# Performance work log

Hardware: AMD Instinct MI355X
Metric: run time of the kernel (lower is better)

The kernel has to match this reference:

```python
import jax, jax.numpy as jnp
import numpy as np

CHUNK = 32


def l2norm(x):
    return x * jax.lax.rsqrt(jnp.sum(x * x, -1, keepdims=True) + 1e-6)


def causal_dwconv(x, w):
    # x: (b, l, C), w: (C, 1, k) -- depthwise causal 1D conv (left pad k-1)
    k = w.shape[-1]
    xt = jnp.transpose(x, (0, 2, 1))
    xt = jnp.pad(xt, ((0, 0), (0, 0), (k - 1, 0)))
    y = jax.lax.conv_general_dilated(xt, w, (1,), 'VALID',
                                     dimension_numbers=('NCH', 'OIH', 'NCH'),
                                     feature_group_count=xt.shape[1])
    return jnp.transpose(y, (0, 2, 1))


def delta_rule_chunkwise(q, k, v, beta):
    # q,k: (b,h,L,dk), v: (b,h,L,dv), beta: (b,h,L). L must be divisible by CHUNK.
    b, h, L, dk = q.shape
    dv = v.shape[-1]
    n = L // CHUNK
    q = l2norm(q)
    k = l2norm(k)
    v = v * beta[..., None]
    kb = k * beta[..., None]
    resh = lambda t: t.reshape(b, h, n, CHUNK, t.shape[-1])
    q, k, v, kb = (resh(t) for t in (q, k, v, kb))
    strict = jnp.tril(jnp.ones((CHUNK, CHUNK), bool), -1)
    A = jnp.where(strict, -(kb @ jnp.swapaxes(k, -1, -2)), 0.0)
    eye = jnp.eye(CHUNK, dtype=A.dtype)
    # UT transform: the sequential forward-substitution loop computes T = (I - A)^{-1}
    T = jax.scipy.linalg.solve_triangular(eye - A, jnp.broadcast_to(eye, A.shape), lower=True)
    u = T @ v
    w = T @ kb
    incl = jnp.tril(jnp.ones((CHUNK, CHUNK), bool))  # lower incl. diag

    def step(S, xs):
        q_i, k_i, u_i, w_i = xs
        attn = jnp.where(incl, q_i @ jnp.swapaxes(k_i, -1, -2), 0.0)
        u_hat = u_i - w_i @ S
        o_i = q_i @ S + attn @ u_hat
        return S + jnp.swapaxes(k_i, -1, -2) @ u_hat, o_i

    xs = tuple(jnp.moveaxis(t, 2, 0) for t in (q, k, u, w))
    S0 = jnp.zeros((b, h, dk, dv), q.dtype)
    S, o = jax.lax.scan(step, S0, xs)
    o = jnp.moveaxis(o, 0, 2).reshape(b, h, L, dv)
    return o, S


def branch_stats(x):
    # per-head stats over the feature dim: mean, std(ddof=1), mean|x|, L2 norm
    m = jnp.mean(x, -1, keepdims=True)
    s = jnp.std(x, -1, keepdims=True, ddof=1)
    a = jnp.mean(jnp.abs(x), -1, keepdims=True)
    l = jnp.sqrt(jnp.sum(x * x, -1, keepdims=True))
    return jnp.concatenate([m, s, a, l], -1)


def reference(hidden_states, q_w, k_w, v_w, b_w, qc_w, kc_w, vc_w,
              fir_w1, fir_w3, fir_w7, fir_w31,
              mlp_w1, mlp_b1, mlp_w2, mlp_b2, gate_log_temp, onorm_w, o_w):
    B, L, D = hidden_states.shape
    H = gate_log_temp.shape[0]
    dk = q_w.shape[1] // H
    dv = v_w.shape[1] // H
    # projections + causal short conv + silu
    q = jax.nn.silu(causal_dwconv(hidden_states @ q_w, qc_w))
    k = jax.nn.silu(causal_dwconv(hidden_states @ k_w, kc_w))
    v = jax.nn.silu(causal_dwconv(hidden_states @ v_w, vc_w))
    q = q.reshape(B, L, H, dk)
    k = k.reshape(B, L, H, dk)
    v_direct = v.reshape(B, L, H, dv)
    beta = jax.nn.sigmoid(hidden_states @ b_w)  # (B,L,H)
    delta_out, _ = delta_rule_chunkwise(
        jnp.transpose(q, (0, 2, 1, 3)), jnp.transpose(k, (0, 2, 1, 3)),
        jnp.transpose(v_direct, (0, 2, 1, 3)), jnp.transpose(beta, (0, 2, 1)))
    delta_out = jnp.transpose(delta_out, (0, 2, 1, 3))  # (B,L,H,dv)
    # multi-scale depthwise FIR branches on v
    v_flat = v_direct.reshape(B, L, H * dv)
    firs = [causal_dwconv(v_flat, w).reshape(B, L, H, dv)
            for w in (fir_w1, fir_w3, fir_w7, fir_w31)]
    branches = firs + [delta_out, v_direct]  # num_streams = 6
    S = len(branches)
    stats = jnp.concatenate([branch_stats(x) for x in branches], -1)  # (B,L,H,S*4)
    gate_in = jnp.concatenate([hidden_states, stats.reshape(B, L, H * S * 4)], -1)
    hgate = jax.nn.gelu(gate_in @ mlp_w1 + mlp_b1, approximate=False)
    logits = (hgate @ mlp_w2 + mlp_b2).reshape(B, L, H, S)
    temp = jax.nn.softplus(gate_log_temp) + 0.5  # min_gate_temp = 0.5
    weights = jax.nn.softmax(logits / temp[None, None, :, None], axis=-1)
    fused = sum(weights[..., i, None] * br for i, br in enumerate(branches))
    # RMSNorm over head_v_dim (eps=1e-5)
    fused = fused * jax.lax.rsqrt(jnp.mean(fused * fused, -1, keepdims=True) + 1e-5) * onorm_w
    return fused.reshape(B, L, H * dv) @ o_w


def setup_inputs() -> dict:
    key = jax.random.key(0)
    B, L, D, H = 2, 2048, 1024, 4
    dk = dv = D // H
    S = 6
    ks = iter(jax.random.split(key, 32))
    nrm = lambda shape, s=0.02: jax.random.normal(next(ks), shape, jnp.float32) * s

    def fir(kw):
        # delta init (last tap = 1) plus small noise
        base = jnp.zeros((H * dv, 1, kw), jnp.float32).at[:, 0, -1].set(1.0)
        return base + nrm((H * dv, 1, kw))

    gate_in_dim = D + S * 4 * H  # 1120
    hgd = D * 2 // 2             # 1024
    b2 = np.zeros(H * S, np.float32)
    for h in range(H):
        b2[h * S + S - 1] = 2.0  # value_bias_init on direct-value stream
    return {
        'hidden_states': jax.random.normal(next(ks), (B, L, D), jnp.float32),
        'q_w': nrm((D, D)), 'k_w': nrm((D, D)), 'v_w': nrm((D, D)),
        'b_w': nrm((D, H)),
        'qc_w': nrm((D, 1, 4), 0.3), 'kc_w': nrm((D, 1, 4), 0.3), 'vc_w': nrm((D, 1, 4), 0.3),
        'fir_w1': fir(1), 'fir_w3': fir(3), 'fir_w7': fir(7), 'fir_w31': fir(31),
        'mlp_w1': nrm((gate_in_dim, hgd)), 'mlp_b1': jnp.zeros((hgd,), jnp.float32),
        'mlp_w2': nrm((hgd, H * S)), 'mlp_b2': jnp.asarray(b2),
        'gate_log_temp': jnp.zeros((H,), jnp.float32),
        'onorm_w': jnp.ones((dv,), jnp.float32),
        'o_w': nrm((D, D)),
    }
```

## Files before the change

### kernel.cpp

```cpp
#include <hip/hip_runtime.h>
#include <hip/hip_bf16.h>
#include <math.h>

#define B_ 2
#define L_ 2048
#define D_ 1024
#define H_ 4
#define NC 64

typedef unsigned short ushort_t;
typedef __bf16 bf16x8 __attribute__((ext_vector_type(8)));
typedef float f32x4 __attribute__((ext_vector_type(4)));
typedef ushort_t u16x8 __attribute__((ext_vector_type(8)));

__device__ __forceinline__ ushort_t f2bs(float f) {
    __hip_bfloat16 h = __float2bfloat16(f);
    ushort_t u;
    __builtin_memcpy(&u, &h, 2);
    return u;
}

__device__ __forceinline__ float wred(float v) {
    v += __shfl_down(v, 32);
    v += __shfl_down(v, 16);
    v += __shfl_down(v, 8);
    v += __shfl_down(v, 4);
    v += __shfl_down(v, 2);
    v += __shfl_down(v, 1);
    return v;
}

__device__ __forceinline__ void gload16(const void* g, void* l) {
    __builtin_amdgcn_global_load_lds((const __attribute__((address_space(1))) void*)g,
                                     (__attribute__((address_space(3))) void*)l, 16, 0, 0);
}

#define LGKM0_BAR()                                          \
    do {                                                     \
        asm volatile("s_waitcnt lgkmcnt(0)" ::: "memory");   \
        __builtin_amdgcn_s_barrier();                        \
    } while (0)

__global__ __launch_bounds__(256) void tcast_k(const float* __restrict__ W,
                                               ushort_t* __restrict__ WT, int K, int N) {
    __shared__ float tile[32 * 33];
    const int k0 = blockIdx.y << 5, n0 = blockIdx.x << 5;
    for (int e = threadIdx.x; e < 1024; e += 256)
        tile[(e >> 5) * 33 + (e & 31)] = W[(size_t)(k0 + (e >> 5)) * N + n0 + (e & 31)];
    __syncthreads();
    for (int e = threadIdx.x; e < 1024; e += 256)
        WT[(size_t)(n0 + (e >> 5)) * K + k0 + (e & 31)] = f2bs(tile[(e & 31) * 33 + (e >> 5)]);
}

__global__ __launch_bounds__(256) void cast_k(const float* __restrict__ x,
                                              ushort_t* __restrict__ y) {
    const int i = blockIdx.x * 256 + threadIdx.x;
    const float4 v = *(const float4*)&x[(size_t)i * 4];
    ushort4 p;
    p.x = f2bs(v.x); p.y = f2bs(v.y); p.z = f2bs(v.z); p.w = f2bs(v.w);
    *(ushort4*)&y[(size_t)i * 4] = p;
}

template <int ACT>
__global__ __launch_bounds__(256) void gemm_bf(const ushort_t* __restrict__ A,
                                               const ushort_t* __restrict__ Bt,
                                               const float* __restrict__ bias,
                                               float* __restrict__ C,
                                               int M, int N, int K) {
    __shared__ ushort_t As[128 * 32];
    __shared__ ushort_t Bs[128 * 32];
    const int t = threadIdx.x;
    const int wv = t >> 6, l = t & 63;
    const int m0 = blockIdx.y << 7, n0 = blockIdx.x << 7;
    const int wm = wv & 1, wn = wv >> 1;
    const int q4 = l >> 4, c16 = l & 15;
    f32x4 acc[4][4];
#pragma unroll
    for (int i = 0; i < 4; ++i)
#pragma unroll
        for (int j = 0; j < 4; ++j) {
            f32x4 z = {0.f, 0.f, 0.f, 0.f};
            acc[i][j] = z;
        }
    const int srow = (l >> 2);
    const int scol = (l & 3) << 3;
    for (int k0 = 0; k0 < K; k0 += 32) {
        __syncthreads();
#pragma unroll
        for (int si = 0; si < 2; ++si) {
            const int s = wv * 2 + si;
            gload16(&A[(size_t)(m0 + s * 16 + srow) * K + k0 + scol], &As[s * 512]);
            gload16(&Bt[(size_t)(n0 + s * 16 + srow) * K + k0 + scol], &Bs[s * 512]);
        }
        __syncthreads();
        bf16x8 af[4], bff[4];
#pragma unroll
        for (int mi = 0; mi < 4; ++mi)
            af[mi] = *(const bf16x8*)&As[(wm * 64 + mi * 16 + c16) * 32 + q4 * 8];
#pragma unroll
        for (int ni = 0; ni < 4; ++ni)
            bff[ni] = *(const bf16x8*)&Bs[(wn * 64 + ni * 16 + c16) * 32 + q4 * 8];
#pragma unroll
        for (int mi = 0; mi < 4; ++mi)
#pragma unroll
            for (int ni = 0; ni < 4; ++ni)
                acc[mi][ni] = __builtin_amdgcn_mfma_f32_16x16x32_bf16(af[mi], bff[ni],
                                                                     acc[mi][ni], 0, 0, 0);
    }
#pragma unroll
    for (int mi = 0; mi < 4; ++mi)
#pragma unroll
        for (int ni = 0; ni < 4; ++ni)
#pragma unroll
            for (int r = 0; r < 4; ++r) {
                const int row = m0 + wm * 64 + mi * 16 + q4 * 4 + r;
                const int col = n0 + wn * 64 + ni * 16 + c16;
                float v = acc[mi][ni][r];
                if (ACT == 1) {
                    v += bias[col];
                    v = 0.5f * v * (1.0f + erff(v * 0.70710678118654752f));
                }
                C[(size_t)row * N + col] = v;
            }
}

template <int DO_NORM, int EMIT_F32, int EMIT_BF>
__global__ __launch_bounds__(256) void convql_k(const float* __restrict__ X,
                                                const float* __restrict__ cw,
                                                float* __restrict__ Y,
                                                ushort_t* __restrict__ Ybf) {
    __shared__ float xs[35 * 256];
    const int bid = blockIdx.x;
    const int h = bid & 3, lt = (bid >> 2) & 63, b = bid >> 8;
    const int t = threadIdx.x;
    const int l0 = lt << 5;
    const int cg = (h << 8) | t;
    for (int e = t; e < 35 * 256; e += 256) {
        const int r = e >> 8, c = e & 255;
        const int gl = l0 + r - 3;
        xs[e] = (gl >= 0) ? X[((size_t)(b * L_) + gl) * 3072 + (h << 8) + c] : 0.f;
    }
    const float w0 = cw[cg * 4 + 0], w1 = cw[cg * 4 + 1];
    const float w2 = cw[cg * 4 + 2], w3 = cw[cg * 4 + 3];
    __syncthreads();
    float yr[32];
#pragma unroll
    for (int l = 0; l < 32; ++l) {
        const float a = xs[(l + 0) * 256 + t] * w0 + xs[(l + 1) * 256 + t] * w1 +
                        xs[(l + 2) * 256 + t] * w2 + xs[(l + 3) * 256 + t] * w3;
        yr[l] = a / (1.f + expf(-a));
    }
    if (DO_NORM) {
        __syncthreads();
#pragma unroll
        for (int l = 0; l < 32; ++l) xs[l * 256 + t] = yr[l];
        __syncthreads();
        const int wv = t >> 6, lane = t & 63;
#pragma unroll
        for (int ri = 0; ri < 8; ++ri) {
            const int r = wv * 8 + ri;
            float4 v = *(float4*)&xs[r * 256 + lane * 4];
            float ss = v.x * v.x + v.y * v.y + v.z * v.z + v.w * v.w;
            ss = wred(ss);
            ss = __shfl(ss, 0);
            const float s = rsqrtf(ss + 1e-6f);
            v.x *= s; v.y *= s; v.z *= s; v.w *= s;
            const size_t go = ((size_t)(b * L_) + l0 + r) * 1024 + (h << 8) + lane * 4;
            if (EMIT_F32) *(float4*)&Y[go] = v;
            if (EMIT_BF) {
                ushort4 p;
                p.x = f2bs(v.x); p.y = f2bs(v.y); p.z = f2bs(v.z); p.w = f2bs(v.w);
                *(ushort4*)&Ybf[go] = p;
            }
        }
    } else {
#pragma unroll
        for (int l = 0; l < 32; ++l)
            if (EMIT_F32) Y[((size_t)(b * L_) + l0 + l) * 1024 + cg] = yr[l];
    }
}

__global__ __launch_bounds__(256) void fir_k(const float* __restrict__ V,
                                             const float* __restrict__ w1w,
                                             const float* __restrict__ w3w,
                                             const float* __restrict__ w7w,
                                             const float* __restrict__ w31w,
                                             float* __restrict__ o1,
                                             float* __restrict__ o3,
                                             float* __restrict__ o7,
                                             float* __restrict__ o31) {
    __shared__ float xs[62 * 256];
    const int bid = blockIdx.x;
    const int h = bid & 3, lt = (bid >> 2) & 63, b = bid >> 8;
    const int t = threadIdx.x;
    const int l0 = lt << 5;
    const int cg = (h << 8) | t;
    for (int e = t; e < 62 * 256; e += 256) {
        const int r = e >> 8, c = e & 255;
        const int gl = l0 + r - 30;
        xs[e] = (gl >= 0) ? V[((size_t)(b * L_) + gl) * 1024 + (h << 8) + c] : 0.f;
    }
    float lw31[31], lw7[7], lw3[3];
#pragma unroll
    for (int j = 0; j < 31; ++j) lw31[j] = w31w[cg * 31 + j];
#pragma unroll
    for (int j = 0; j < 7; ++j) lw7[j] = w7w[cg * 7 + j];
#pragma unroll
    for (int j = 0; j < 3; ++j) lw3[j] = w3w[cg * 3 + j];
    const float lw1 = w1w[cg];
    __syncthreads();
    for (int l = 0; l < 32; ++l) {
        float a31 = 0.f, a7 = 0.f, a3 = 0.f, v = 0.f;
#pragma unroll
        for (int j = 0; j < 31; ++j) {
            v = xs[(l + j) * 256 + t];
            a31 += v * lw31[j];
            if (j >= 24) a7 += v * lw7[j - 24];
            if (j >= 28) a3 += v * lw3[j - 28];
        }
        const size_t go = ((size_t)(b * L_) + l0 + l) * 1024 + cg;
        o31[go] = a31;
        o7[go] = a7;
        o3[go] = a3;
        o1[go] = v * lw1;
    }
}

__global__ __launch_bounds__(64) void beta_k(const float* __restrict__ hs,
                                             const float* __restrict__ bw,
                                             float* __restrict__ beta,
                                             ushort_t* __restrict__ gin) {
    const int row = blockIdx.x;
    const int lane = threadIdx.x;
    float a0 = 0, a1 = 0, a2 = 0, a3 = 0;
    const float* hp = hs + (size_t)row * D_;
    ushort_t* gp = gin + (size_t)row * 1120;
    for (int c = lane; c < D_; c += 64) {
        const float x = hp[c];
        gp[c] = f2bs(x);
        a0 += x * bw[c * 4 + 0];
        a1 += x * bw[c * 4 + 1];
        a2 += x * bw[c * 4 + 2];
        a3 += x * bw[c * 4 + 3];
    }
    a0 = wred(a0); a1 = wred(a1); a2 = wred(a2); a3 = wred(a3);
    if (lane == 0) {
        float* o = beta + (size_t)row * 4;
        o[0] = 1.f / (1.f + expf(-a0));
        o[1] = 1.f / (1.f + expf(-a1));
        o[2] = 1.f / (1.f + expf(-a2));
        o[3] = 1.f / (1.f + expf(-a3));
    }
}

__global__ __launch_bounds__(256) void prep2_k(const ushort_t* __restrict__ qbf,
                                               const ushort_t* __restrict__ kbf,
                                               const float* __restrict__ vg,
                                               const float* __restrict__ beta,
                                               ushort_t* __restrict__ qfr,
                                               ushort_t* __restrict__ wfr,
                                               float* __restrict__ ufr,
                                               ushort_t* __restrict__ atfr,
                                               ushort_t* __restrict__ ktfr) {
    __shared__ ushort_t k_lds[32 * 264];
    __shared__ ushort_t kT_lds[256 * 32];
    __shared__ ushort_t vT_lds[256 * 32];
    __shared__ float Am[32 * 33];
    __shared__ float Tm[32 * 33];
    __shared__ ushort_t Tb[32 * 40];
    __shared__ ushort_t at_s[32 * 40];
    __shared__ float beta_s[32];
    const int bid = blockIdx.x;
    const int bh = bid >> 6, ci = bid & 63;
    const int b = bh >> 2, h = bh & 3;
    const int t = threadIdx.x;
    const int wv = t >> 6, lane = t & 63;
    const int mi = wv & 1, ni = wv >> 1;
    const int l16 = lane & 15, quad = lane >> 4;
    const size_t cb = (size_t)bid;
    const size_t grow = ((size_t)(b * L_ + ci * 32)) * 1024 + (h << 8);
    const f32x4 z4 = {0.f, 0.f, 0.f, 0.f};

    if (t < 32) beta_s[t] = beta[(size_t)(b * L_ + ci * 32 + t) * 4 + h];
#pragma unroll
    for (int j = 0; j < 4; ++j) {
        const int idx = j * 2048 + t * 8, r = idx >> 8, c = idx & 255;
        *(u16x8*)&k_lds[r * 264 + c] = *(const u16x8*)&kbf[grow + (size_t)r * 1024 + c];
    }
#pragma unroll
    for (int j = 0; j < 8; ++j) {
        const int e = j * 1024 + t * 4, r = e >> 8, c = e & 255;
        const float4 v4 = *(const float4*)&vg[grow + (size_t)r * 1024 + c];
        const float vv[4] = {v4.x, v4.y, v4.z, v4.w};
#pragma unroll
        for (int x = 0; x < 4; ++x) {
            const int cc = c + x;
            const int sp = (r >> 3) ^ ((cc >> 1) & 3);
            vT_lds[cc * 32 + sp * 8 + (r & 7)] = f2bs(vv[x]);
        }
    }
    f32x4 g = z4, atv = z4;
#pragma unroll
    for (int s = 0; s < 8; ++s) {
        const bf16x8 a =
            *(const bf16x8*)&kbf[grow + (size_t)(mi * 16 + l16) * 1024 + s * 32 + (quad << 3)];
        const bf16x8 bb =
            *(const bf16x8*)&kbf[grow + (size_t)(ni * 16 + l16) * 1024 + s * 32 + (quad << 3)];
        const bf16x8 qa =
            *(const bf16x8*)&qbf[grow + (size_t)(mi * 16 + l16) * 1024 + s * 32 + (quad << 3)];
        g = __builtin_amdgcn_mfma_f32_16x16x32_bf16(a, bb, g, 0, 0, 0);
        atv = __builtin_amdgcn_mfma_f32_16x16x32_bf16(qa, bb, atv, 0, 0, 0);
        if (ni == 0) *(bf16x8*)&qfr[((cb * 2 + mi) * 8 + s) * 512 + lane * 8] = qa;
    }
    __syncthreads();
#pragma unroll
    for (int r = 0; r < 4; ++r) {
        const int row = mi * 16 + (quad << 2) + r;
        const int col = ni * 16 + l16;
        Am[row * 33 + col] = (col < row) ? -beta_s[row] * g[r] : 0.f;
        Tm[row * 33 + col] = (row == col) ? 1.f : 0.f;
        at_s[row * 40 + col] = (col <= row) ? f2bs(atv[r]) : (ushort_t)0;
    }
#pragma unroll
    for (int j = 0; j < 8; ++j) {
        const int e = j * 1024 + t * 4, r = e >> 8, c = e & 255;
#pragma unroll
        for (int x = 0; x < 4; ++x) {
            const int cc = c + x;
            const int sp = (r >> 3) ^ ((cc >> 1) & 3);
            kT_lds[cc * 32 + sp * 8 + (r & 7)] = k_lds[r * 264 + cc];
        }
    }
    __syncthreads();
    if (wv < 2) {
        const u16x8 av = *(const u16x8*)&at_s[(wv * 16 + l16) * 40 + (quad << 3)];
        *(u16x8*)&atfr[(cb * 2 + wv) * 512 + lane * 8] = av;
    }
#pragma unroll
    for (int j2 = 0; j2 < 4; ++j2) {
        const int tc = wv * 4 + j2;
        const int c = tc * 16 + l16;
        const int sp = quad ^ ((c >> 1) & 3);
        *(u16x8*)&ktfr[(cb * 16 + tc) * 512 + lane * 8] = *(const u16x8*)&kT_lds[c * 32 + sp * 8];
    }
    for (int i = 1; i < 32; ++i) {
        if (t < 32) {
            float s = 0.f;
            for (int j = 0; j < i; ++j) s += Am[i * 33 + j] * Tm[j * 33 + t];
            Tm[i * 33 + t] += s;
        }
        __syncthreads();
    }
#pragma unroll
    for (int j = 0; j < 4; ++j) {
        const int e = j * 256 + t, i = e >> 5, jj = e & 31;
        Tb[i * 40 + jj] = f2bs(Tm[i * 33 + jj] * beta_s[jj]);
    }
    __syncthreads();
    const bf16x8 tf = *(const bf16x8*)&Tb[(mi * 16 + l16) * 40 + (quad << 3)];
#pragma unroll
    for (int j = 0; j < 8; ++j) {
        const int nt = ni * 8 + j;
        const int d = (nt << 4) + l16;
        const int sp = quad ^ ((d >> 1) & 3);
        const bf16x8 kb = *(const bf16x8*)&kT_lds[d * 32 + (sp << 3)];
        const bf16x8 vb = *(const bf16x8*)&vT_lds[d * 32 + (sp << 3)];
        const f32x4 wacc = __builtin_amdgcn_mfma_f32_16x16x32_bf16(tf, kb, z4, 0, 0, 0);
        const f32x4 uacc = __builtin_amdgcn_mfma_f32_16x16x32_bf16(tf, vb, z4, 0, 0, 0);
        *(float4*)&ufr[((cb * 16 + nt) * 2 + mi) * 256 + lane * 4] =
            make_float4(uacc[0], uacc[1], uacc[2], uacc[3]);
#pragma unroll
        for (int r = 0; r < 4; ++r) {
            const int row = mi * 16 + (quad << 2) + r;
            k_lds[row * 264 + d] = f2bs(wacc[r]);
        }
    }
    __syncthreads();
    if (wv < 2) {
#pragma unroll
        for (int s = 0; s < 8; ++s) {
            const u16x8 wv8 = *(const u16x8*)&k_lds[(wv * 16 + l16) * 264 + s * 32 + (quad << 3)];
            *(u16x8*)&wfr[((cb * 2 + wv) * 8 + s) * 512 + lane * 8] = wv8;
        }
    }
}

__global__ __launch_bounds__(256, 1) void scan5_k(const ushort_t* __restrict__ qfr,
                                                  const ushort_t* __restrict__ wfr,
                                                  const float* __restrict__ ufr,
                                                  const ushort_t* __restrict__ atfr,
                                                  const ushort_t* __restrict__ ktfr,
                                                  float* __restrict__ dlt) {
    __shared__ ushort_t uh_lds[16 * 40];
    __shared__ ushort_t S_lds[2][16 * 264];
    const int t = threadIdx.x;
    const int wv = t >> 6, lane = t & 63;
    const int bh = blockIdx.x & 7, tile = blockIdx.x >> 3;
    const int b = bh >> 2, h = bh & 3;
    const int l16 = lane & 15, quad = lane >> 4;
    for (int e = t; e < 16 * 264; e += 256) S_lds[0][e] = 0;

    f32x4 Sacc[8];
#pragma unroll
    for (int j = 0; j < 8; ++j) {
        f32x4 z = {0.f, 0.f, 0.f, 0.f};
        Sacc[j] = z;
    }

    bf16x8 wfA[8], qfA[8], atfA, ktA[8];
    bf16x8 wfB[8], qfB[8], atfB, ktB[8];
    float uvA[4], uvB[4];

    auto loadf = [&](int ci, bf16x8* wf, bf16x8* qf, bf16x8& atf, float* uv, bf16x8* ktf) {
        const size_t cb = (size_t)(bh * NC + ci);
        if (wv < 2) {
            const ushort_t* wsrc = wfr + (cb * 2 + wv) * 8 * 512;
            const ushort_t* qsrc = qfr + (cb * 2 + wv) * 8 * 512;
#pragma unroll
            for (int s = 0; s < 8; ++s) {
                wf[s] = *(const bf16x8*)&wsrc[s * 512 + lane * 8];
                qf[s] = *(const bf16x8*)&qsrc[s * 512 + lane * 8];
            }
            atf = *(const bf16x8*)&atfr[(cb * 2 + wv) * 512 + lane * 8];
            const float4 u4 = *(const float4*)&ufr[((cb * 16 + tile) * 2 + wv) * 256 + lane * 4];
            uv[0] = u4.x; uv[1] = u4.y; uv[2] = u4.z; uv[3] = u4.w;
        } else {
            const ushort_t* ksrc = ktfr + cb * 16 * 512;
#pragma unroll
            for (int j = 0; j < 8; ++j) {
                const int tc = ((wv - 2) << 3) + j;
                ktf[j] = *(const bf16x8*)&ksrc[tc * 512 + lane * 8];
            }
        }
    };
    auto sfrag = [&](int p, int k0) -> bf16x8 {
        return *(const bf16x8*)&S_lds[p][l16 * 264 + k0 + (quad << 3)];
    };
    auto uhfrag = [&]() -> bf16x8 {
        return *(const bf16x8*)&uh_lds[l16 * 40 + (quad << 3)];
    };
    auto compute = [&](int ci, bf16x8* wf, bf16x8* qf, bf16x8& atf, float* uv, bf16x8* ktf) {
        const int p = ci & 1;
        const size_t gbase = ((size_t)(b * L_ + ci * 32)) * D_ + (h << 8);
        if (wv < 2) {
            f32x4 a0 = {0.f, 0.f, 0.f, 0.f}, a1 = {0.f, 0.f, 0.f, 0.f};
#pragma unroll
            for (int s = 0; s < 8; s += 2) {
                a0 = __builtin_amdgcn_mfma_f32_16x16x32_bf16(wf[s], sfrag(p, s * 32), a0, 0, 0, 0);
                a1 = __builtin_amdgcn_mfma_f32_16x16x32_bf16(wf[s + 1], sfrag(p, s * 32 + 32), a1,
                                                             0, 0, 0);
            }
            ushort4 up;
            up.x = f2bs(uv[0] - a0[0] - a1[0]);
            up.y = f2bs(uv[1] - a0[1] - a1[1]);
            up.z = f2bs(uv[2] - a0[2] - a1[2]);
            up.w = f2bs(uv[3] - a0[3] - a1[3]);
            *(ushort4*)&uh_lds[l16 * 40 + (wv << 4) + (quad << 2)] = up;
        }
        LGKM0_BAR();
        if (wv < 2) {
            f32x4 o0 = {0.f, 0.f, 0.f, 0.f}, o1 = {0.f, 0.f, 0.f, 0.f};
#pragma unroll
            for (int s = 0; s < 8; s += 2) {
                o0 = __builtin_amdgcn_mfma_f32_16x16x32_bf16(qf[s], sfrag(p, s * 32), o0, 0, 0, 0);
                o1 = __builtin_amdgcn_mfma_f32_16x16x32_bf16(qf[s + 1], sfrag(p, s * 32 + 32), o1,
                                                             0, 0, 0);
            }
            o0 = __builtin_amdgcn_mfma_f32_16x16x32_bf16(atf, uhfrag(), o0, 0, 0, 0);
#pragma unroll
            for (int r = 0; r < 4; ++r)
                dlt[gbase + (size_t)((wv << 4) + (quad << 2) + r) * D_ + (tile << 4) + l16] =
                    o0[r] + o1[r];
        } else {
            const bf16x8 uf = uhfrag();
#pragma unroll
            for (int j = 0; j < 8; ++j)
                Sacc[j] = __builtin_amdgcn_mfma_f32_16x16x32_bf16(ktf[j], uf, Sacc[j], 0, 0, 0);
#pragma unroll
            for (int j = 0; j < 8; ++j) {
                const int c0 = ((((wv - 2) << 3) + j) << 4) + (quad << 2);
                ushort4 pk;
                pk.x = f2bs(Sacc[j][0]);
                pk.y = f2bs(Sacc[j][1]);
                pk.z = f2bs(Sacc[j][2]);
                pk.w = f2bs(Sacc[j][3]);
                *(ushort4*)&S_lds[p ^ 1][l16 * 264 + c0] = pk;
            }
        }
        LGKM0_BAR();
    };

    loadf(0, wfA, qfA, atfA, uvA, ktA);
    LGKM0_BAR();
    for (int ci = 0; ci < NC; ci += 2) {
        loadf(ci + 1, wfB, qfB, atfB, uvB, ktB);
        compute(ci, wfA, qfA, atfA, uvA, ktA);
        if (ci + 2 < NC) loadf(ci + 2, wfA, qfA, atfA, uvA, ktA);
        compute(ci + 1, wfB, qfB, atfB, uvB, ktB);
    }
}

__global__ __launch_bounds__(64) void stats_k(const float* __restrict__ f1,
                                              const float* __restrict__ f3,
                                              const float* __restrict__ f7,
                                              const float* __restrict__ f31,
                                              const float* __restrict__ dl,
                                              const float* __restrict__ vv,
                                              ushort_t* __restrict__ gin) {
    const int row = blockIdx.x;
    const int lane = threadIdx.x;
    const float* ptrs[6] = {f1, f3, f7, f31, dl, vv};
    const size_t base = (size_t)row * 256;
    ushort_t* gp = gin + (size_t)(row >> 2) * 1120 + 1024 + (row & 3) * 24;
    for (int br = 0; br < 6; ++br) {
        const float4 x = *(const float4*)&ptrs[br][base + lane * 4];
        float s1 = x.x + x.y + x.z + x.w;
        float s2 = x.x * x.x + x.y * x.y + x.z * x.z + x.w * x.w;
        float sa = fabsf(x.x) + fabsf(x.y) + fabsf(x.z) + fabsf(x.w);
        s1 = wred(s1); s2 = wred(s2); sa = wred(sa);
        if (lane == 0) {
            const float m = s1 / 256.f;
            float var = (s2 - 256.f * m * m) / 255.f;
            if (var < 0.f) var = 0.f;
            gp[br * 4 + 0] = f2bs(m);
            gp[br * 4 + 1] = f2bs(sqrtf(var));
            gp[br * 4 + 2] = f2bs(sa / 256.f);
            gp[br * 4 + 3] = f2bs(sqrtf(s2));
        }
    }
}

__global__ __launch_bounds__(256) void wts_k(const float* __restrict__ hg,
                                             const float* __restrict__ w2,
                                             const float* __restrict__ b2,
                                             const float* __restrict__ glt,
                                             float* __restrict__ wts) {
    const int row = blockIdx.x;
    const int h = threadIdx.x >> 6, lane = threadIdx.x & 63;
    float hv[16];
    const float* hp = hg + (size_t)row * 1024;
#pragma unroll
    for (int ii = 0; ii < 16; ++ii) hv[ii] = hp[lane + 64 * ii];
    float lg[6];
#pragma unroll
    for (int s = 0; s < 6; ++s) {
        const int j = h * 6 + s;
        float acc = 0.f;
#pragma unroll
        for (int ii = 0; ii < 16; ++ii) acc += hv[ii] * w2[(size_t)(lane + 64 * ii) * 24 + j];
        lg[s] = wred(acc);
    }
    if (lane == 0) {
        const float temp = log1pf(expf(glt[h])) + 0.5f;
        float mx = -1e30f;
#pragma unroll
        for (int s = 0; s < 6; ++s) {
            lg[s] = (lg[s] + b2[h * 6 + s]) / temp;
            mx = fmaxf(mx, lg[s]);
        }
        float se = 0.f;
#pragma unroll
        for (int s = 0; s < 6; ++s) {
            lg[s] = expf(lg[s] - mx);
            se += lg[s];
        }
        float* o = &wts[(size_t)row * 24 + h * 6];
        const float inv = 1.f / se;
#pragma unroll
        for (int s = 0; s < 6; ++s) o[s] = lg[s] * inv;
    }
}

__global__ __launch_bounds__(1024) void fuse_k(const float* __restrict__ f1,
                                               const float* __restrict__ f3,
                                               const float* __restrict__ f7,
                                               const float* __restrict__ f31,
                                               const float* __restrict__ dl,
                                               const float* __restrict__ vv,
                                               const float* __restrict__ wts,
                                               const float* __restrict__ onw,
                                               ushort_t* __restrict__ fused) {
    __shared__ float wloc[24];
    __shared__ float psum[16];
    const int row = blockIdx.x, t = threadIdx.x;
    if (t < 24) wloc[t] = wts[(size_t)row * 24 + t];
    __syncthreads();
    const int h = t >> 8, dd = t & 255;
    const size_t idx = (size_t)row * 1024 + t;
    const float* ptrs[6] = {f1, f3, f7, f31, dl, vv};
    float f = 0.f;
#pragma unroll
    for (int br = 0; br < 6; ++br) f += wloc[h * 6 + br] * ptrs[br][idx];
    float ss = wred(f * f);
    const int wave = t >> 6;
    if ((t & 63) == 0) psum[wave] = ss;
    __syncthreads();
    const float tot = psum[h * 4 + 0] + psum[h * 4 + 1] + psum[h * 4 + 2] + psum[h * 4 + 3];
    const float scale = rsqrtf(tot / 256.f + 1e-5f);
    fused[idx] = f2bs(f * scale * onw[dd]);
}

extern "C" void kernel_launch(void* const* d_in, const int* in_sizes, int n_in,
                              void* d_out, int out_size, void* d_ws, size_t ws_size,
                              hipStream_t stream) {
    const float* hs   = (const float*)d_in[0];
    const float* q_w  = (const float*)d_in[1];
    const float* k_w  = (const float*)d_in[2];
    const float* v_w  = (const float*)d_in[3];
    const float* b_w  = (const float*)d_in[4];
    const float* qc_w = (const float*)d_in[5];
    const float* kc_w = (const float*)d_in[6];
    const float* vc_w = (const float*)d_in[7];
    const float* f1w  = (const float*)d_in[8];
    const float* f3w  = (const float*)d_in[9];
    const float* f7w  = (const float*)d_in[10];
    const float* f31w = (const float*)d_in[11];
    const float* w1   = (const float*)d_in[12];
    const float* b1   = (const float*)d_in[13];
    const float* w2   = (const float*)d_in[14];
    const float* b2   = (const float*)d_in[15];
    const float* glt  = (const float*)d_in[16];
    const float* onw  = (const float*)d_in[17];
    const float* o_w  = (const float*)d_in[18];
    float* out = (float*)d_out;

    const size_t SZ = (size_t)B_ * L_ * D_;
    float* qlin = (float*)d_ws;
    float* klin = qlin + SZ;
    float* vlin = klin + SZ;
    float* qbuf = vlin + SZ;
    float* kbuf = qbuf + SZ;
    float* vbuf = kbuf + SZ;
    float* f31b = vbuf + SZ;
    float* wb   = f31b + SZ;
    float* ub   = wb + SZ;
    float* dlt  = ub + SZ;
    float* beta = dlt + SZ;
    float* attn = beta + (size_t)B_ * L_ * H_;
    float* f1b = qlin;
    float* f3b = klin;
    float* f7b = vlin;
    float* hgate = kbuf;
    float* qkv = qlin;
    float* wts = attn + (size_t)B_ * H_ * NC * 1024;

    ushort_t* hs_bf = (ushort_t*)dlt;
    ushort_t* qwT = (ushort_t*)f31b;
    ushort_t* kwT = (ushort_t*)f31b + 1048576;
    ushort_t* vwT = (ushort_t*)f31b + 2097152;
    ushort_t* qbf = (ushort_t*)f31b + 3145728;
    ushort_t* kbf = (ushort_t*)kbuf;
    ushort_t* gin_bf = (ushort_t*)qbuf;
    ushort_t* w1T = (ushort_t*)(wb + 2359296);
    ushort_t* owT = (ushort_t*)ub;
    ushort_t* fused_bf = (ushort_t*)kbuf;
    ushort_t* ktfr = (ushort_t*)klin;
    ushort_t* qfr = (ushort_t*)klin + SZ;
    ushort_t* wfr = (ushort_t*)wb;
    float* ufr = ub;
    ushort_t* atfr = (ushort_t*)attn;

    const int M = B_ * L_;

    tcast_k<<<dim3(32, 32), 256, 0, stream>>>(q_w, qwT, 1024, 1024);
    tcast_k<<<dim3(32, 32), 256, 0, stream>>>(k_w, kwT, 1024, 1024);
    tcast_k<<<dim3(32, 32), 256, 0, stream>>>(v_w, vwT, 1024, 1024);
    cast_k<<<4096, 256, 0, stream>>>(hs, hs_bf);
    gemm_bf<0><<<dim3(24, 32), 256, 0, stream>>>(hs_bf, qwT, nullptr, qkv, M, 3072, 1024);
    beta_k<<<M, 64, 0, stream>>>(hs, b_w, beta, gin_bf);
    convql_k<1, 0, 1><<<512, 256, 0, stream>>>(qkv + 0,    qc_w, nullptr, qbf);
    convql_k<1, 0, 1><<<512, 256, 0, stream>>>(qkv + 1024, kc_w, nullptr, kbf);
    convql_k<0, 1, 0><<<512, 256, 0, stream>>>(qkv + 2048, vc_w, vbuf, nullptr);
    prep2_k<<<B_ * H_ * NC, 256, 0, stream>>>(qbf, kbf, vbuf, beta, qfr, wfr, ufr, atfr, ktfr);
    scan5_k<<<128, 256, 0, stream>>>(qfr, wfr, ufr, atfr, ktfr, dlt);
    fir_k<<<512, 256, 0, stream>>>(vbuf, f1w, f3w, f7w, f31w, f1b, f3b, f7b, f31b);
    stats_k<<<M * H_, 64, 0, stream>>>(f1b, f3b, f7b, f31b, dlt, vbuf, gin_bf);
    tcast_k<<<dim3(32, 35), 256, 0, stream>>>(w1, w1T, 1120, 1024);
    gemm_bf<1><<<dim3(8, 32), 256, 0, stream>>>(gin_bf, w1T, b1, hgate, M, 1024, 1120);
    wts_k<<<M, 256, 0, stream>>>(hgate, w2, b2, glt, wts);
    fuse_k<<<M, 1024, 0, stream>>>(f1b, f3b, f7b, f31b, dlt, vbuf, wts, onw, fused_bf);
    tcast_k<<<dim3(32, 32), 256, 0, stream>>>(o_w, owT, 1024, 1024);
    gemm_bf<0><<<dim3(8, 32), 256, 0, stream>>>(fused_bf, owT, nullptr, out, M, 1024, 1024);
}
```

Measured before the change: 604.4 us.

## Collapse chunk scan into a single wavefront to drop per-chunk barriers

Replaces the 4-wave scan kernel with a single 64-thread wave per block that does the W·S, Q·S, state update and intra-chunk attention itself. This removes the two block barriers per chunk and keeps the S state in one wave's registers and LDS. Q fragments are now staged into LDS through async global-to-LDS loads, prefetched one chunk ahead. In exchange each block has a quarter of the threads and a longer serial MFMA chain per chunk, so latency hiding is reduced and register pressure rises.

```diff
diff --git a/kernel.cpp b/kernel.cpp
--- a/kernel.cpp
+++ b/kernel.cpp
@@ -34,12 +34,6 @@
     __builtin_amdgcn_global_load_lds((const __attribute__((address_space(1))) void*)g,
                                      (__attribute__((address_space(3))) void*)l, 16, 0, 0);
 }
-
-#define LGKM0_BAR()                                          \
-    do {                                                     \
-        asm volatile("s_waitcnt lgkmcnt(0)" ::: "memory");   \
-        __builtin_amdgcn_s_barrier();                        \
-    } while (0)
 
 __global__ __launch_bounds__(256) void tcast_k(const float* __restrict__ W,
                                                ushort_t* __restrict__ WT, int K, int N) {
@@ -385,118 +379,124 @@
     }
 }
 
-__global__ __launch_bounds__(256, 1) void scan5_k(const ushort_t* __restrict__ qfr,
-                                                  const ushort_t* __restrict__ wfr,
-                                                  const float* __restrict__ ufr,
-                                                  const ushort_t* __restrict__ atfr,
-                                                  const ushort_t* __restrict__ ktfr,
-                                                  float* __restrict__ dlt) {
-    __shared__ ushort_t uh_lds[16 * 40];
-    __shared__ ushort_t S_lds[2][16 * 264];
-    const int t = threadIdx.x;
-    const int wv = t >> 6, lane = t & 63;
+__global__ __launch_bounds__(64, 1) void scan6_k(const ushort_t* __restrict__ qfr,
+                                                 const ushort_t* __restrict__ wfr,
+                                                 const float* __restrict__ ufr,
+                                                 const ushort_t* __restrict__ atfr,
+                                                 const ushort_t* __restrict__ ktfr,
+                                                 float* __restrict__ dlt) {
+    __shared__ ushort_t qstg[2][16 * 512];
+    __shared__ ushort_t Sm[8 * 512];
+    __shared__ ushort_t uhL[512];
+    const int l = threadIdx.x;
+    const int q = l >> 4, c = l & 15;
     const int bh = blockIdx.x & 7, tile = blockIdx.x >> 3;
     const int b = bh >> 2, h = bh & 3;
-    const int l16 = lane & 15, quad = lane >> 4;
-    for (int e = t; e < 16 * 264; e += 256) S_lds[0][e] = 0;
-
-    f32x4 Sacc[8];
-#pragma unroll
-    for (int j = 0; j < 8; ++j) {
+
+    const int4 z16 = {0, 0, 0, 0};
+#pragma unroll
+    for (int e = 0; e < 8; ++e) *(int4*)&Sm[(e * 64 + l) * 8] = z16;
+
+    f32x4 Sacc[16];
+#pragma unroll
+    for (int tc = 0; tc < 16; ++tc) {
         f32x4 z = {0.f, 0.f, 0.f, 0.f};
-        Sacc[j] = z;
-    }
-
-    bf16x8 wfA[8], qfA[8], atfA, ktA[8];
-    bf16x8 wfB[8], qfB[8], atfB, ktB[8];
-    float uvA[4], uvB[4];
-
-    auto loadf = [&](int ci, bf16x8* wf, bf16x8* qf, bf16x8& atf, float* uv, bf16x8* ktf) {
+        Sacc[tc] = z;
+    }
+
+    bf16x8 wA[2][8], wB[2][8], atA[2], atB[2], ktf[16];
+    float4 uA[2], uB[2];
+
+    auto loadf = [&](int ci, bf16x8 (*wf)[8], bf16x8* atf, float4* uf, ushort_t* qdst) {
         const size_t cb = (size_t)(bh * NC + ci);
-        if (wv < 2) {
-            const ushort_t* wsrc = wfr + (cb * 2 + wv) * 8 * 512;
-            const ushort_t* qsrc = qfr + (cb * 2 + wv) * 8 * 512;
-#pragma unroll
-            for (int s = 0; s < 8; ++s) {
-                wf[s] = *(const bf16x8*)&wsrc[s * 512 + lane * 8];
-                qf[s] = *(const bf16x8*)&qsrc[s * 512 + lane * 8];
+        const ushort_t* qsrc = qfr + cb * (2 * 8 * 512);
+#pragma unroll
+        for (int f = 0; f < 16; ++f)
+            gload16(&qsrc[f * 512 + l * 8], &qdst[f * 512]);
+        const ushort_t* wsrc = wfr + cb * (2 * 8 * 512);
+#pragma unroll
+        for (int hf = 0; hf < 2; ++hf)
+#pragma unroll
+            for (int s = 0; s < 8; ++s)
+                wf[hf][s] = *(const bf16x8*)&wsrc[(hf * 8 + s) * 512 + l * 8];
+#pragma unroll
+        for (int hf = 0; hf < 2; ++hf) {
+            atf[hf] = *(const bf16x8*)&atfr[(cb * 2 + hf) * 512 + l * 8];
+            uf[hf] = *(const float4*)&ufr[((cb * 16 + tile) * 2 + hf) * 256 + l * 4];
+        }
+    };
+
+    auto computef = [&](int ci, bf16x8 (*wf)[8], bf16x8* atf, float4* uf,
+                        const ushort_t* qsp, int pci, bf16x8 (*pwf)[8], bf16x8* patf,
+                        float4* puf, ushort_t* pqd) {
+        asm volatile("s_waitcnt vmcnt(0)" ::: "memory");
+        __builtin_amdgcn_sched_barrier(0);
+        const size_t cb = (size_t)(bh * NC + ci);
+        const ushort_t* ksrc = ktfr + cb * (16 * 512);
+#pragma unroll
+        for (int tc = 0; tc < 16; ++tc)
+            ktf[tc] = *(const bf16x8*)&ksrc[tc * 512 + l * 8];
+        if (pci < NC) loadf(pci, pwf, patf, puf, pqd);
+
+        f32x4 aw0[2], aw1[2], oq0[2], oq1[2];
+#pragma unroll
+        for (int hf = 0; hf < 2; ++hf) {
+            f32x4 z = {0.f, 0.f, 0.f, 0.f};
+            aw0[hf] = z; aw1[hf] = z; oq0[hf] = z; oq1[hf] = z;
+        }
+#pragma unroll
+        for (int s = 0; s < 8; ++s) {
+            const bf16x8 Sb = *(const bf16x8*)&Sm[(s * 64 + l) * 8];
+            const bf16x8 q0 = *(const bf16x8*)&qsp[(0 * 8 + s) * 512 + l * 8];
+            const bf16x8 q1 = *(const bf16x8*)&qsp[(1 * 8 + s) * 512 + l * 8];
+            if (s & 1) {
+                aw1[0] = __builtin_amdgcn_mfma_f32_16x16x32_bf16(wf[0][s], Sb, aw1[0], 0, 0, 0);
+                aw1[1] = __builtin_amdgcn_mfma_f32_16x16x32_bf16(wf[1][s], Sb, aw1[1], 0, 0, 0);
+                oq1[0] = __builtin_amdgcn_mfma_f32_16x16x32_bf16(q0, Sb, oq1[0], 0, 0, 0);
+                oq1[1] = __builtin_amdgcn_mfma_f32_16x16x32_bf16(q1, Sb, oq1[1], 0, 0, 0);
+            } else {
+                aw0[0] = __builtin_amdgcn_mfma_f32_16x16x32_bf16(wf[0][s], Sb, aw0[0], 0, 0, 0);
+                aw0[1] = __builtin_amdgcn_mfma_f32_16x16x32_bf16(wf[1][s], Sb, aw0[1], 0, 0, 0);
+                oq0[0] = __builtin_amdgcn_mfma_f32_16x16x32_bf16(q0, Sb, oq0[0], 0, 0, 0);
+                oq0[1] = __builtin_amdgcn_mfma_f32_16x16x32_bf16(q1, Sb, oq0[1], 0, 0, 0);
             }
-            atf = *(const bf16x8*)&atfr[(cb * 2 + wv) * 512 + lane * 8];
-            const float4 u4 = *(const float4*)&ufr[((cb * 16 + tile) * 2 + wv) * 256 + lane * 4];
-            uv[0] = u4.x; uv[1] = u4.y; uv[2] = u4.z; uv[3] = u4.w;
-        } else {
-            const ushort_t* ksrc = ktfr + cb * 16 * 512;
-#pragma unroll
-            for (int j = 0; j < 8; ++j) {
-                const int tc = ((wv - 2) << 3) + j;
-                ktf[j] = *(const bf16x8*)&ksrc[tc * 512 + lane * 8];
-            }
-        }
+        }
+#pragma unroll
+        for (int hf = 0; hf < 2; ++hf) {
+            const float4 uv = uf[hf];
+            ushort4 up;
+            up.x = f2bs(uv.x - aw0[hf][0] - aw1[hf][0]);
+            up.y = f2bs(uv.y - aw0[hf][1] - aw1[hf][1]);
+            up.z = f2bs(uv.z - aw0[hf][2] - aw1[hf][2]);
+            up.w = f2bs(uv.w - aw0[hf][3] - aw1[hf][3]);
+            *(ushort4*)&uhL[((2 * hf + (q >> 1)) * 16 + c) * 8 + (q & 1) * 4] = up;
+        }
+        const bf16x8 uhB = *(const bf16x8*)&uhL[l * 8];
+#pragma unroll
+        for (int tc = 0; tc < 16; ++tc) {
+            Sacc[tc] = __builtin_amdgcn_mfma_f32_16x16x32_bf16(ktf[tc], uhB, Sacc[tc], 0, 0, 0);
+            ushort4 pk;
+            pk.x = f2bs(Sacc[tc][0]);
+            pk.y = f2bs(Sacc[tc][1]);
+            pk.z = f2bs(Sacc[tc][2]);
+            pk.w = f2bs(Sacc[tc][3]);
+            *(ushort4*)&Sm[(((tc >> 1) * 64) + ((tc & 1) * 2 + (q >> 1)) * 16 + c) * 8 +
+                           (q & 1) * 4] = pk;
+        }
+        oq0[0] = __builtin_amdgcn_mfma_f32_16x16x32_bf16(atf[0], uhB, oq0[0], 0, 0, 0);
+        oq0[1] = __builtin_amdgcn_mfma_f32_16x16x32_bf16(atf[1], uhB, oq0[1], 0, 0, 0);
+        const size_t gbase = ((size_t)(b * L_ + ci * 32)) * 1024 + (h << 8) + (tile << 4) + c;
+#pragma unroll
+        for (int hf = 0; hf < 2; ++hf)
+#pragma unroll
+            for (int r = 0; r < 4; ++r)
+                dlt[gbase + (size_t)(hf * 16 + (q << 2) + r) * 1024] = oq0[hf][r] + oq1[hf][r];
     };
-    auto sfrag = [&](int p, int k0) -> bf16x8 {
-        return *(const bf16x8*)&S_lds[p][l16 * 264 + k0 + (quad << 3)];
-    };
-    auto uhfrag = [&]() -> bf16x8 {
-        return *(const bf16x8*)&uh_lds[l16 * 40 + (quad << 3)];
-    };
-    auto compute = [&](int ci, bf16x8* wf, bf16x8* qf, bf16x8& atf, float* uv, bf16x8* ktf) {
-        const int p = ci & 1;
-        const size_t gbase = ((size_t)(b * L_ + ci * 32)) * D_ + (h << 8);
-        if (wv < 2) {
-            f32x4 a0 = {0.f, 0.f, 0.f, 0.f}, a1 = {0.f, 0.f, 0.f, 0.f};
-#pragma unroll
-            for (int s = 0; s < 8; s += 2) {
-                a0 = __builtin_amdgcn_mfma_f32_16x16x32_bf16(wf[s], sfrag(p, s * 32), a0, 0, 0, 0);
-                a1 = __builtin_amdgcn_mfma_f32_16x16x32_bf16(wf[s + 1], sfrag(p, s * 32 + 32), a1,
-                                                             0, 0, 0);
-            }
-            ushort4 up;
-            up.x = f2bs(uv[0] - a0[0] - a1[0]);
-            up.y = f2bs(uv[1] - a0[1] - a1[1]);
-            up.z = f2bs(uv[2] - a0[2] - a1[2]);
-            up.w = f2bs(uv[3] - a0[3] - a1[3]);
-            *(ushort4*)&uh_lds[l16 * 40 + (wv << 4) + (quad << 2)] = up;
-        }
-        LGKM0_BAR();
-        if (wv < 2) {
-            f32x4 o0 = {0.f, 0.f, 0.f, 0.f}, o1 = {0.f, 0.f, 0.f, 0.f};
-#pragma unroll
-            for (int s = 0; s < 8; s += 2) {
-                o0 = __builtin_amdgcn_mfma_f32_16x16x32_bf16(qf[s], sfrag(p, s * 32), o0, 0, 0, 0);
-                o1 = __builtin_amdgcn_mfma_f32_16x16x32_bf16(qf[s + 1], sfrag(p, s * 32 + 32), o1,
-                                                             0, 0, 0);
-            }
-            o0 = __builtin_amdgcn_mfma_f32_16x16x32_bf16(atf, uhfrag(), o0, 0, 0, 0);
-#pragma unroll
-            for (int r = 0; r < 4; ++r)
-                dlt[gbase + (size_t)((wv << 4) + (quad << 2) + r) * D_ + (tile << 4) + l16] =
-                    o0[r] + o1[r];
-        } else {
-            const bf16x8 uf = uhfrag();
-#pragma unroll
-            for (int j = 0; j < 8; ++j)
-                Sacc[j] = __builtin_amdgcn_mfma_f32_16x16x32_bf16(ktf[j], uf, Sacc[j], 0, 0, 0);
-#pragma unroll
-            for (int j = 0; j < 8; ++j) {
-                const int c0 = ((((wv - 2) << 3) + j) << 4) + (quad << 2);
-                ushort4 pk;
-                pk.x = f2bs(Sacc[j][0]);
-                pk.y = f2bs(Sacc[j][1]);
-                pk.z = f2bs(Sacc[j][2]);
-                pk.w = f2bs(Sacc[j][3]);
-                *(ushort4*)&S_lds[p ^ 1][l16 * 264 + c0] = pk;
-            }
-        }
-        LGKM0_BAR();
-    };
-
-    loadf(0, wfA, qfA, atfA, uvA, ktA);
-    LGKM0_BAR();
+
+    loadf(0, wA, atA, uA, &qstg[0][0]);
     for (int ci = 0; ci < NC; ci += 2) {
-        loadf(ci + 1, wfB, qfB, atfB, uvB, ktB);
-        compute(ci, wfA, qfA, atfA, uvA, ktA);
-        if (ci + 2 < NC) loadf(ci + 2, wfA, qfA, atfA, uvA, ktA);
-        compute(ci + 1, wfB, qfB, atfB, uvB, ktB);
+        computef(ci, wA, atA, uA, &qstg[0][0], ci + 1, wB, atB, uB, &qstg[1][0]);
+        computef(ci + 1, wB, atB, uB, &qstg[1][0], ci + 2, wA, atA, uA, &qstg[0][0]);
     }
 }
 
@@ -672,7 +672,7 @@
     convql_k<1, 0, 1><<<512, 256, 0, stream>>>(qkv + 1024, kc_w, nullptr, kbf);
     convql_k<0, 1, 0><<<512, 256, 0, stream>>>(qkv + 2048, vc_w, vbuf, nullptr);
     prep2_k<<<B_ * H_ * NC, 256, 0, stream>>>(qbf, kbf, vbuf, beta, qfr, wfr, ufr, atfr, ktfr);
-    scan5_k<<<128, 256, 0, stream>>>(qfr, wfr, ufr, atfr, ktfr, dlt);
+    scan6_k<<<128, 64, 0, stream>>>(qfr, wfr, ufr, atfr, ktfr, dlt);
     fir_k<<<512, 256, 0, stream>>>(vbuf, f1w, f3w, f7w, f31w, f1b, f3b, f7b, f31b);
     stats_k<<<M * H_, 64, 0, stream>>>(f1b, f3b, f7b, f31b, dlt, vbuf, gin_bf);
     tcast_k<<<dim3(32, 35), 256, 0, stream>>>(w1, w1T, 1120, 1024);
```

Result: faster. 582.4 us (-3.6%).
